# Performance work log

Measured on AMD Instinct MI355X. Metric: run time of the kernel, lower is better.

## Reference

```python
import jax, jax.numpy as jnp
import numpy as np


def setup_inputs() -> dict:
    key = jax.random.key(0)
    ks = jax.random.split(key, 9)
    B, C, H, W = 8, 512, 56, 56
    E = 256  # embed_dim = in_channels / r
    s = 0.02
    return {
        "x": jax.random.normal(ks[0], (B, C, H, W), dtype=jnp.float32),
        "wq": jax.random.normal(ks[1], (E, C), dtype=jnp.float32) * s,
        "bq": jax.random.normal(ks[2], (E,), dtype=jnp.float32) * s,
        "wk": jax.random.normal(ks[3], (E, C), dtype=jnp.float32) * s,
        "bk": jax.random.normal(ks[4], (E,), dtype=jnp.float32) * s,
        "wv": jax.random.normal(ks[5], (E, C), dtype=jnp.float32) * s,
        "bv": jax.random.normal(ks[6], (E,), dtype=jnp.float32) * s,
        "wo": jax.random.normal(ks[7], (C, E), dtype=jnp.float32) * s,
        "bo": jax.random.normal(ks[8], (C,), dtype=jnp.float32) * s,
    }


def reference(x, wq, bq, wk, bk, wv, bv, wo, bo):
    B, C, H, W = x.shape
    N = H * W
    # 1x1 convs == per-pixel linear projections; flatten spatial dims
    xf = x.reshape(B, C, N)                                   # b c n
    q = jnp.einsum("ec,bcn->bne", wq, xf) + bq                # b n e
    k = jnp.einsum("ec,bcn->ben", wk, xf) + bk[None, :, None] # b e n
    v = jnp.einsum("ec,bcn->bne", wv, xf) + bv                # b n e
    attn = jnp.einsum("bne,bem->bnm", q, k) / N               # b n n (unnormalized, /N scale)
    embed = jnp.einsum("bnm,bme->bne", attn, v)               # b n e
    out = jnp.einsum("ce,bne->bcn", wo, embed) + bo[None, :, None]
    return out.reshape(B, C, H, W) + x
```

## Files before the change

### kernel.cpp

```cpp
#include <hip/hip_runtime.h>
#include <hip/hip_bf16.h>


typedef __attribute__((ext_vector_type(8))) __bf16 bf16x8;
typedef __attribute__((ext_vector_type(4))) float floatx4;

struct __align__(8) bh4 { __hip_bfloat16 x, y, z, w; };
struct __align__(16) bh8 { __hip_bfloat16 h[8]; };

__device__ __forceinline__ void load_lds16(const void* g, void* l) {
    __builtin_amdgcn_global_load_lds((const __attribute__((address_space(1))) void*)g,
                                     (__attribute__((address_space(3))) void*)l, 16, 0, 0);
}

__global__ __launch_bounds__(256)
void prep_trans(const float* __restrict__ x, __hip_bfloat16* __restrict__ xT,
                __hip_bfloat16* __restrict__ xnp, float* __restrict__ s,
                const float* __restrict__ wo, const float* __restrict__ wv,
                const float* __restrict__ wq, const float* __restrict__ wk,
                const float* __restrict__ bq, const float* __restrict__ bk,
                const float* __restrict__ bv,
                __hip_bfloat16* __restrict__ Pdb, __hip_bfloat16* __restrict__ Qtb,
                float* __restrict__ u, float* __restrict__ r, float* __restrict__ w,
                float* __restrict__ kap)
{
    __shared__ __align__(16) float smem[64 * 65];
    const int tid = threadIdx.x;

    if (blockIdx.z == 8) {
        const int blk = blockIdx.y * 50 + blockIdx.x;
        if (blk >= 131) return;
        if (blk >= 128) {
            int blk2 = blk - 128;
            if (blk2 < 2) {
                int c = blk2 * 256 + tid;
                float su = 0.f, sr = 0.f, sw = 0.f;
                for (int e = 0; e < 256; ++e) {
                    su = fmaf(wo[(long long)c * 256 + e], bv[e], su);
                    sr = fmaf(bk[e], wq[(long long)e * 512 + c], sr);
                    sw = fmaf(wk[(long long)e * 512 + c], bq[e], sw);
                }
                u[c] = su; r[c] = sr; w[c] = sw;
                if (c == 0) {
                    float k2 = 0.f;
                    for (int e = 0; e < 256; ++e) k2 = fmaf(bk[e], bq[e], k2);
                    *kap = k2;
                }
            } else {
                float4* p = (float4*)s;
                for (int i = tid; i < 1024; i += 256) p[i] = make_float4(0.f, 0.f, 0.f, 0.f);
            }
            return;
        }
        const bool doQ = (blk >= 64);
        const int tt = blk & 63;
        const int m0 = (tt >> 3) * 64, n0 = (tt & 7) * 64;
        float (*As)[68] = (float(*)[68])smem;
        float (*Bs)[68] = (float(*)[68])(smem + 16 * 68);
        const int tx = tid & 15, ty = tid >> 4;
        const int lk = tid >> 4, lc = (tid & 15) * 4;
        const int lr = tid >> 2, lk4 = (tid & 3) * 4;
        float acc[4][4] = {};
        for (int k0 = 0; k0 < 256; k0 += 16) {
            float4 av, bv4;
            if (doQ) {
                av = *(const float4*)&wq[(long long)(k0 + lk) * 512 + m0 + lc];
                bv4 = *(const float4*)&wk[(long long)(k0 + lk) * 512 + n0 + lc];
            } else {
                av = *(const float4*)&wo[(long long)(m0 + lr) * 256 + k0 + lk4];
                bv4 = *(const float4*)&wv[(long long)(k0 + lk) * 512 + n0 + lc];
            }
            __syncthreads();
            if (doQ) {
                *(float4*)&As[lk][lc] = av;
            } else {
                As[lk4 + 0][lr] = av.x; As[lk4 + 1][lr] = av.y;
                As[lk4 + 2][lr] = av.z; As[lk4 + 3][lr] = av.w;
            }
            *(float4*)&Bs[lk][lc] = bv4;
            __syncthreads();
#pragma unroll
            for (int kk = 0; kk < 16; ++kk) {
                float a[4], b[4];
#pragma unroll
                for (int i = 0; i < 4; ++i) { a[i] = As[kk][ty * 4 + i]; b[i] = Bs[kk][tx * 4 + i]; }
#pragma unroll
                for (int i = 0; i < 4; ++i)
#pragma unroll
                    for (int j = 0; j < 4; ++j) acc[i][j] = fmaf(a[i], b[j], acc[i][j]);
            }
        }
        const int mo = m0 + ty * 4, no = n0 + tx * 4;
        if (doQ) {
#pragma unroll
            for (int i = 0; i < 4; ++i)
#pragma unroll
                for (int j = 0; j < 4; ++j)
                    Qtb[(long long)(mo + i) * 512 + no + j] = __float2bfloat16(acc[i][j]);
        } else {
#pragma unroll
            for (int i = 0; i < 4; ++i)
#pragma unroll
                for (int j = 0; j < 4; ++j) {
                    __hip_bfloat16 v = __float2bfloat16(acc[i][j]);
                    Pdb[(long long)(mo + i) * 1024 + no + j] = v;
                    Pdb[(long long)(mo + i) * 1024 + no + j + 512] = v;
                }
        }
        return;
    }

    float (*t)[65] = (float(*)[65])smem;
    const int b = blockIdx.z;
    const int n0 = blockIdx.x * 64, c0 = blockIdx.y * 64;
    const int nch = tid & 7;
    const int cr  = tid >> 3;
    __hip_bfloat16* xTo = xT + (long long)b * 3200 * 512;
    __hip_bfloat16* xno = xnp + (long long)b * 512 * 3200;

    if (n0 >= 3136) {
        bh8 z8;
#pragma unroll
        for (int k = 0; k < 8; ++k) z8.h[k] = __float2bfloat16(0.f);
#pragma unroll
        for (int pass = 0; pass < 2; ++pass) {
            int rr = cr + 32 * pass;
            *(bh8*)&xno[(long long)(c0 + rr) * 3200 + n0 + nch * 8] = z8;
            *(bh8*)&xTo[(long long)(n0 + rr) * 512 + c0 + nch * 8] = z8;
        }
        return;
    }
    const float* xb = x + (long long)b * 512 * 3136;
#pragma unroll
    for (int pass = 0; pass < 2; ++pass) {
        const int cl = cr + 32 * pass;
        const int c = c0 + cl;
        const float* xr = xb + (long long)c * 3136 + n0 + nch * 8;
        float4 v0 = *(const float4*)xr;
        float4 v1 = *(const float4*)(xr + 4);
        bh8 o;
        o.h[0] = __float2bfloat16(v0.x); o.h[1] = __float2bfloat16(v0.y);
        o.h[2] = __float2bfloat16(v0.z); o.h[3] = __float2bfloat16(v0.w);
        o.h[4] = __float2bfloat16(v1.x); o.h[5] = __float2bfloat16(v1.y);
        o.h[6] = __float2bfloat16(v1.z); o.h[7] = __float2bfloat16(v1.w);
        *(bh8*)&xno[(long long)c * 3200 + n0 + nch * 8] = o;
        const int nl = nch * 8;
        t[nl + 0][cl] = v0.x; t[nl + 1][cl] = v0.y;
        t[nl + 2][cl] = v0.z; t[nl + 3][cl] = v0.w;
        t[nl + 4][cl] = v1.x; t[nl + 5][cl] = v1.y;
        t[nl + 6][cl] = v1.z; t[nl + 7][cl] = v1.w;
        float rs = v0.x + v0.y + v0.z + v0.w + v1.x + v1.y + v1.z + v1.w;
        rs += __shfl_xor(rs, 1, 8);
        rs += __shfl_xor(rs, 2, 8);
        rs += __shfl_xor(rs, 4, 8);
        if (nch == 0) atomicAdd(&s[b * 512 + c], rs);
    }
    __syncthreads();
#pragma unroll
    for (int pass = 0; pass < 2; ++pass) {
        const int nl = cr + 32 * pass;
        const int cc = nch * 8;
        bh8 o;
#pragma unroll
        for (int k = 0; k < 8; ++k) o.h[k] = __float2bfloat16(t[nl][cc + k]);
        *(bh8*)&xTo[(long long)(n0 + nl) * 512 + c0 + cc] = o;
    }
}

__global__ __launch_bounds__(256)
void vec2_kernel(const __hip_bfloat16* __restrict__ T, const __hip_bfloat16* __restrict__ Pdb,
                 const __hip_bfloat16* __restrict__ Qtb, const float* __restrict__ s,
                 const float* __restrict__ u, const float* __restrict__ w,
                 const float* __restrict__ kap, const float* __restrict__ bo,
                 float* __restrict__ ps, float* __restrict__ sq, float* __restrict__ a2)
{
    const int idx = blockIdx.x * 4 + (threadIdx.x >> 6);
    const int lane = threadIdx.x & 63;
    const int b = idx >> 9, c = idx & 511;
    const int j0 = lane * 8;
    const float* sb = s + b * 512;
    float4 s0 = *(const float4*)&sb[j0], s1 = *(const float4*)&sb[j0 + 4];
    float4 w0 = *(const float4*)&w[j0],  w1 = *(const float4*)&w[j0 + 4];
    bf16x8 pv = *(const bf16x8*)&Pdb[(long long)c * 1024 + j0];
    bf16x8 qv = *(const bf16x8*)&Qtb[(long long)c * 512 + j0];
    bf16x8 tv = *(const bf16x8*)&T[(long long)b * 262144 + (long long)c * 512 + j0];
    float sj[8] = {s0.x, s0.y, s0.z, s0.w, s1.x, s1.y, s1.z, s1.w};
    float wj[8] = {w0.x, w0.y, w0.z, w0.w, w1.x, w1.y, w1.z, w1.w};
    float aps = 0.f, asq = 0.f, atw = 0.f, asw = 0.f;
#pragma unroll
    for (int t = 0; t < 8; ++t) {
        aps = fmaf((float)pv[t], sj[t], aps);
        asq = fmaf((float)qv[t], sj[t], asq);
        atw = fmaf((float)tv[t], wj[t], atw);
        asw = fmaf(sj[t], wj[t], asw);
    }
#pragma unroll
    for (int m = 1; m < 64; m <<= 1) {
        aps += __shfl_xor(aps, m);
        asq += __shfl_xor(asq, m);
        atw += __shfl_xor(atw, m);
        asw += __shfl_xor(asw, m);
    }
    if (lane == 0) {
        ps[idx] = aps; sq[idx] = asq;
        float kp = *kap;
        a2[idx] = (atw + u[c] * asw + aps * kp) * (1.f / 3136.f) + u[c] * kp + bo[c];
    }
}

#define SWZ64(row) ((row) & 7)

__global__ __launch_bounds__(256)
void mfma_g(const __hip_bfloat16* __restrict__ A, long long sA, int lda,
            __hip_bfloat16* __restrict__ C, long long sC, int ldc,
            int kLen)
{
    constexpr int BKT = 64;
    constexpr int CPR = BKT / 8;
    constexpr int NC = 64 * CPR / 256;
    constexpr int LSZ = 64 * BKT;
    __shared__ __hip_bfloat16 As[2 * LSZ];
    __shared__ __hip_bfloat16 Bs[2 * LSZ];
    const int tid = threadIdx.x;
    const int lane = tid & 63;
    const int w = tid >> 6;
    const int wm = (w >> 1) << 5;
    const int wn = (w & 1) << 5;
    const int ln = lane & 15;
    const int hi = lane >> 4;
    const int bx = blockIdx.x;
    const int batch = bx & 7, ks = bx >> 3;
    int p = blockIdx.y, mt = 0;
    while (p >= 8 - mt) { p -= 8 - mt; ++mt; }
    const int nt = mt + p;
    const int m0 = mt << 6, n0 = nt << 6;
    const long long k0 = (long long)ks * kLen;

    const __hip_bfloat16* gA[NC];
    const __hip_bfloat16* gB[NC];
#pragma unroll
    for (int q0 = 0; q0 < NC; ++q0) {
        int q = tid + 256 * q0;
        int row = q / CPR;
        int c = (q % CPR) ^ SWZ64(row);
        gA[q0] = A + batch * sA + (long long)(m0 + row) * lda + k0 + c * 8;
        gB[q0] = A + batch * sA + (long long)(n0 + row) * lda + k0 + c * 8;
    }
    floatx4 acc[2][2] = {};
    const int nK = kLen / BKT;

#pragma unroll
    for (int q0 = 0; q0 < NC; ++q0) {
        load_lds16(gA[q0], As + (tid + 256 * q0) * 8);
        load_lds16(gB[q0], Bs + (tid + 256 * q0) * 8);
        gA[q0] += BKT; gB[q0] += BKT;
    }

    int cur = 0;
    for (int kt = 0; kt < nK; ++kt) {
        if (kt + 1 < nK) {
            const int off = (cur ^ 1) * LSZ;
#pragma unroll
            for (int q0 = 0; q0 < NC; ++q0) {
                load_lds16(gA[q0], As + off + (tid + 256 * q0) * 8);
                load_lds16(gB[q0], Bs + off + (tid + 256 * q0) * 8);
                gA[q0] += BKT; gB[q0] += BKT;
            }
            asm volatile("s_waitcnt vmcnt(4)" ::: "memory");
        } else {
            asm volatile("s_waitcnt vmcnt(0)" ::: "memory");
        }
        __builtin_amdgcn_s_barrier();
        const __hip_bfloat16* Ac = As + cur * LSZ;
        const __hip_bfloat16* Bc = Bs + cur * LSZ;
#pragma unroll
        for (int kk = 0; kk < BKT / 32; ++kk) {
            const int cidx = kk * 4 + hi;
            bf16x8 af[2], bfr[2];
#pragma unroll
            for (int i = 0; i < 2; ++i) {
                int row = wm + i * 16 + ln;
                af[i] = *(const bf16x8*)(Ac + row * BKT + ((cidx ^ SWZ64(row)) << 3));
            }
#pragma unroll
            for (int j = 0; j < 2; ++j) {
                int row = wn + j * 16 + ln;
                bfr[j] = *(const bf16x8*)(Bc + row * BKT + ((cidx ^ SWZ64(row)) << 3));
            }
#pragma unroll
            for (int i = 0; i < 2; ++i)
#pragma unroll
                for (int j = 0; j < 2; ++j)
                    acc[i][j] = __builtin_amdgcn_mfma_f32_16x16x32_bf16(af[i], bfr[j], acc[i][j], 0, 0, 0);
        }
        if (kt + 1 < nK) {
            __builtin_amdgcn_s_barrier();
            cur ^= 1;
        }
    }

    __hip_bfloat16* Cb = C + batch * sC + ks * 512;
#pragma unroll
    for (int i = 0; i < 2; ++i) {
        int mb = m0 + wm + i * 16 + hi * 4;
#pragma unroll
        for (int j = 0; j < 2; ++j) {
            int nl = n0 + wn + j * 16 + ln;
            bh4 mv;
            mv.x = __float2bfloat16(acc[i][j][0]);
            mv.y = __float2bfloat16(acc[i][j][1]);
            mv.z = __float2bfloat16(acc[i][j][2]);
            mv.w = __float2bfloat16(acc[i][j][3]);
            Cb[(long long)(mb + 0) * ldc + nl] = mv.x;
            Cb[(long long)(mb + 1) * ldc + nl] = mv.y;
            Cb[(long long)(mb + 2) * ldc + nl] = mv.z;
            Cb[(long long)(mb + 3) * ldc + nl] = mv.w;
            if (mt != nt)
                *(bh4*)&Cb[(long long)nl * ldc + mb] = mv;
        }
    }
}

template<int MODE>
__global__ __launch_bounds__(256)
void mfma_sm(const __hip_bfloat16* __restrict__ A, long long sA, int lda,
             const __hip_bfloat16* __restrict__ B, long long sB, int ldb,
             __hip_bfloat16* __restrict__ C, long long sC, int ldc,
             const float* __restrict__ pu, const float* __restrict__ pr,
             const float* __restrict__ pps, const float* __restrict__ psq,
             int kLen)
{
    constexpr int BKT = 64;
    constexpr int CPR = BKT / 8;
    constexpr int NC = 64 * CPR / 256;
    constexpr int LSZ = 64 * BKT;
    __shared__ __hip_bfloat16 As[2 * LSZ];
    __shared__ __hip_bfloat16 Bs[2 * LSZ];
    const int tid = threadIdx.x;
    const int lane = tid & 63;
    const int w = tid >> 6;
    const int wm = (w >> 1) << 5;
    const int wn = (w & 1) << 5;
    const int ln = lane & 15;
    const int hi = lane >> 4;
    const int batch = blockIdx.x;
    const int m0 = blockIdx.z << 6;
    const int n0 = blockIdx.y << 6;

    const __hip_bfloat16* gA[NC];
    const __hip_bfloat16* gB[NC];
#pragma unroll
    for (int q0 = 0; q0 < NC; ++q0) {
        int q = tid + 256 * q0;
        int row = q / CPR;
        int c = (q % CPR) ^ SWZ64(row);
        gA[q0] = A + batch * sA + (long long)(m0 + row) * lda + c * 8;
        gB[q0] = B + batch * sB + (long long)(n0 + row) * ldb + c * 8;
    }
    floatx4 acc[2][2] = {};
    const int nK = kLen / BKT;

#pragma unroll
    for (int q0 = 0; q0 < NC; ++q0) {
        load_lds16(gA[q0], As + (tid + 256 * q0) * 8);
        load_lds16(gB[q0], Bs + (tid + 256 * q0) * 8);
        gA[q0] += BKT; gB[q0] += BKT;
    }

    int cur = 0;
    for (int kt = 0; kt < nK; ++kt) {
        if (kt + 1 < nK) {
            const int off = (cur ^ 1) * LSZ;
#pragma unroll
            for (int q0 = 0; q0 < NC; ++q0) {
                load_lds16(gA[q0], As + off + (tid + 256 * q0) * 8);
                load_lds16(gB[q0], Bs + off + (tid + 256 * q0) * 8);
                gA[q0] += BKT; gB[q0] += BKT;
            }
            asm volatile("s_waitcnt vmcnt(4)" ::: "memory");
        } else {
            asm volatile("s_waitcnt vmcnt(0)" ::: "memory");
        }
        __builtin_amdgcn_s_barrier();
        const __hip_bfloat16* Ac = As + cur * LSZ;
        const __hip_bfloat16* Bc = Bs + cur * LSZ;
#pragma unroll
        for (int kk = 0; kk < BKT / 32; ++kk) {
            const int cidx = kk * 4 + hi;
            bf16x8 af[2], bfr[2];
#pragma unroll
            for (int i = 0; i < 2; ++i) {
                int row = wm + i * 16 + ln;
                af[i] = *(const bf16x8*)(Ac + row * BKT + ((cidx ^ SWZ64(row)) << 3));
            }
#pragma unroll
            for (int j = 0; j < 2; ++j) {
                int row = wn + j * 16 + ln;
                bfr[j] = *(const bf16x8*)(Bc + row * BKT + ((cidx ^ SWZ64(row)) << 3));
            }
#pragma unroll
            for (int i = 0; i < 2; ++i)
#pragma unroll
                for (int j = 0; j < 2; ++j)
                    acc[i][j] = __builtin_amdgcn_mfma_f32_16x16x32_bf16(af[i], bfr[j], acc[i][j], 0, 0, 0);
        }
        if (kt + 1 < nK) {
            __builtin_amdgcn_s_barrier();
            cur ^= 1;
        }
    }

    __hip_bfloat16* Cb = C + batch * sC;
#pragma unroll
    for (int i = 0; i < 2; ++i) {
        int mb = m0 + wm + i * 16 + hi * 4;
#pragma unroll
        for (int r = 0; r < 4; ++r) {
#pragma unroll
            for (int j = 0; j < 2; ++j) {
                int nl = n0 + wn + j * 16 + ln;
                float v = acc[i][j][r];
                if (MODE == 6) {
                    float uu = pu[mb + r], rr = pr[nl];
                    v = (v + uu * psq[batch * 512 + nl] + pps[batch * 512 + mb + r] * rr)
                        * (1.f / 3136.f) + uu * rr;
                    if (mb + r == nl) v += 1.f;
                }
                Cb[(long long)(mb + r) * ldc + nl] = __float2bfloat16(v);
            }
        }
    }
}

__global__ __launch_bounds__(256)
void mfma64(const __hip_bfloat16* __restrict__ A, long long sA, int lda,
            const __hip_bfloat16* __restrict__ B, long long sB, int ldb,
            float* __restrict__ C, long long sC, int ldc,
            const float* __restrict__ bias, int sBias,
            int kLen, int Nreal)
{
    constexpr int BKT = 64;
    constexpr int CPR = BKT / 8;
    constexpr int NA = 64 * CPR / 256;
    constexpr int NB = 128 * CPR / 256;
    __shared__ __hip_bfloat16 As[64 * BKT];
    __shared__ __hip_bfloat16 Bs[128 * BKT];
    const int tid = threadIdx.x;
    const int lane = tid & 63;
    const int w = tid >> 6;
    const int ln = lane & 15;
    const int hi = lane >> 4;
    const int batch = blockIdx.x;
    const int m0 = blockIdx.z << 6;
    const int n0 = blockIdx.y << 7;

    const __hip_bfloat16* gA[NA];
    const __hip_bfloat16* gB[NB];
#pragma unroll
    for (int q0 = 0; q0 < NA; ++q0) {
        int q = tid + 256 * q0;
        int row = q / CPR;
        int c = (q % CPR) ^ SWZ64(row);
        gA[q0] = A + batch * sA + (long long)(m0 + row) * lda + c * 8;
    }
#pragma unroll
    for (int q0 = 0; q0 < NB; ++q0) {
        int q = tid + 256 * q0;
        int row = q / CPR;
        int c = (q % CPR) ^ SWZ64(row);
        gB[q0] = B + batch * sB + (long long)(n0 + row) * ldb + c * 8;
    }

    floatx4 acc[4][2] = {};
    const int nK = kLen / BKT;
    for (int kt = 0; kt < nK; ++kt) {
#pragma unroll
        for (int q0 = 0; q0 < NA; ++q0) {
            load_lds16(gA[q0], As + (tid + 256 * q0) * 8);
            gA[q0] += BKT;
        }
#pragma unroll
        for (int q0 = 0; q0 < NB; ++q0) {
            load_lds16(gB[q0], Bs + (tid + 256 * q0) * 8);
            gB[q0] += BKT;
        }
        __syncthreads();
#pragma unroll
        for (int kk = 0; kk < BKT / 32; ++kk) {
            const int cidx = kk * 4 + hi;
            bf16x8 af[4], bfr[2];
#pragma unroll
            for (int i = 0; i < 4; ++i) {
                int row = i * 16 + ln;
                af[i] = *(const bf16x8*)(As + row * BKT + ((cidx ^ SWZ64(row)) << 3));
            }
#pragma unroll
            for (int j = 0; j < 2; ++j) {
                int row = w * 32 + j * 16 + ln;
                bfr[j] = *(const bf16x8*)(Bs + row * BKT + ((cidx ^ SWZ64(row)) << 3));
            }
#pragma unroll
            for (int i = 0; i < 4; ++i)
#pragma unroll
                for (int j = 0; j < 2; ++j)
                    acc[i][j] = __builtin_amdgcn_mfma_f32_16x16x32_bf16(af[i], bfr[j], acc[i][j], 0, 0, 0);
        }
        __syncthreads();
    }

    float* Cb = C + batch * sC;
#pragma unroll
    for (int i = 0; i < 4; ++i) {
        int mb = m0 + i * 16 + hi * 4;
#pragma unroll
        for (int r = 0; r < 4; ++r) {
            float bb = bias[batch * sBias + mb + r];
#pragma unroll
            for (int j = 0; j < 2; ++j) {
                int nl = n0 + w * 32 + j * 16 + ln;
                if (nl < Nreal) {
                    Cb[(long long)(mb + r) * ldc + nl] = acc[i][j][r] + bb;
                }
            }
        }
    }
}

extern "C" void kernel_launch(void* const* d_in, const int* in_sizes, int n_in,
                              void* d_out, int out_size, void* d_ws, size_t ws_size,
                              hipStream_t stream)
{
    const float* x  = (const float*)d_in[0];
    const float* wq = (const float*)d_in[1];
    const float* bq = (const float*)d_in[2];
    const float* wk = (const float*)d_in[3];
    const float* bk = (const float*)d_in[4];
    const float* wv = (const float*)d_in[5];
    const float* bv = (const float*)d_in[6];
    const float* wo = (const float*)d_in[7];
    const float* bo = (const float*)d_in[8];
    float* out = (float*)d_out;

    const int N = 3136;
    const long long xs = 512LL * N;
    const long long xs2 = 512LL * 3200;

    char* ob = (char*)d_out;
    __hip_bfloat16* xnp = (__hip_bfloat16*)ob;
    __hip_bfloat16* Gp2 = (__hip_bfloat16*)(ob + 26214400);
    __hip_bfloat16* Tb  = (__hip_bfloat16*)(ob + 34603008);

    char* wsb = (char*)d_ws;
    __hip_bfloat16* xT  = (__hip_bfloat16*)wsb;
    __hip_bfloat16* A2b = (__hip_bfloat16*)(wsb + 26214400);
    __hip_bfloat16* Pdb = (__hip_bfloat16*)(wsb + 30408704);
    __hip_bfloat16* Qtb = (__hip_bfloat16*)(wsb + 31457280);
    float* sv  = (float*)(wsb + 31981568);
    float* u_  = (float*)(wsb + 31997952);
    float* r_  = (float*)(wsb + 32000000);
    float* w_  = (float*)(wsb + 32002048);
    float* kap = (float*)(wsb + 32004096);
    float* ps  = (float*)(wsb + 32004112);
    float* sq  = (float*)(wsb + 32020496);
    float* a2v = (float*)(wsb + 32036880);

    prep_trans<<<dim3(50, 8, 9), 256, 0, stream>>>(
        x, xT, xnp, sv, wo, wv, wq, wk, bq, bk, bv,
        Pdb, Qtb, u_, r_, w_, kap);

    mfma_g<<<dim3(16, 36), 256, 0, stream>>>(
        xnp, xs2, 3200, Gp2, 524288, 1024, 1600);

    mfma_sm<5><<<dim3(8, 8, 8), 256, 0, stream>>>(
        Pdb, 0, 1024, Gp2, 524288, 1024, Tb, 262144, 512,
        nullptr, nullptr, nullptr, nullptr, 1024);

    vec2_kernel<<<1024, 256, 0, stream>>>(Tb, Pdb, Qtb, sv, u_, w_, kap, bo, ps, sq, a2v);

    mfma_sm<6><<<dim3(8, 8, 8), 256, 0, stream>>>(
        Tb, 262144, 512, Qtb, 0, 512, A2b, 262144, 512,
        u_, r_, ps, sq, 512);

    mfma64<<<dim3(8, 25, 8), 256, 0, stream>>>(
        A2b, 262144, 512, xT, 3200LL * 512, 512,
        out, xs, N, a2v, 512, 512, N);
}
```

Before: 212.8 us.

## Drop transposed x copy; transpose B tile in LDS inside final GEMM

The prep kernel no longer writes a transposed bf16 copy of x (xT), which removes one full-size write of about 26MB and its LDS transpose. The final GEMM now reads the channel-major xnp buffer directly, using register loads and scalar short stores into LDS with a new swizzle instead of async global-to-LDS loads. The zeroing of the row-sum buffer moves from an extra prep block to a hipMemsetAsync, and xnp is relocated into the workspace. The trade-off is a slower B-tile fill in the GEMM: eight scattered 2-byte LDS stores per vector, with possible bank conflicts, and no asynchronous load path.

```diff
diff --git a/kernel.cpp b/kernel.cpp
--- a/kernel.cpp
+++ b/kernel.cpp
@@ -3,6 +3,7 @@
 
 
 typedef __attribute__((ext_vector_type(8))) __bf16 bf16x8;
+typedef __attribute__((ext_vector_type(8))) short s16x8;
 typedef __attribute__((ext_vector_type(4))) float floatx4;
 
 struct __align__(8) bh4 { __hip_bfloat16 x, y, z, w; };
@@ -14,8 +15,8 @@
 }
 
 __global__ __launch_bounds__(256)
-void prep_trans(const float* __restrict__ x, __hip_bfloat16* __restrict__ xT,
-                __hip_bfloat16* __restrict__ xnp, float* __restrict__ s,
+void prep_trans(const float* __restrict__ x, __hip_bfloat16* __restrict__ xnp,
+                float* __restrict__ s,
                 const float* __restrict__ wo, const float* __restrict__ wv,
                 const float* __restrict__ wq, const float* __restrict__ wk,
                 const float* __restrict__ bq, const float* __restrict__ bk,
@@ -24,31 +25,25 @@
                 float* __restrict__ u, float* __restrict__ r, float* __restrict__ w,
                 float* __restrict__ kap)
 {
-    __shared__ __align__(16) float smem[64 * 65];
+    __shared__ __align__(16) float smem[2 * 16 * 68];
     const int tid = threadIdx.x;
 
     if (blockIdx.z == 8) {
         const int blk = blockIdx.y * 50 + blockIdx.x;
-        if (blk >= 131) return;
+        if (blk >= 130) return;
         if (blk >= 128) {
-            int blk2 = blk - 128;
-            if (blk2 < 2) {
-                int c = blk2 * 256 + tid;
-                float su = 0.f, sr = 0.f, sw = 0.f;
-                for (int e = 0; e < 256; ++e) {
-                    su = fmaf(wo[(long long)c * 256 + e], bv[e], su);
-                    sr = fmaf(bk[e], wq[(long long)e * 512 + c], sr);
-                    sw = fmaf(wk[(long long)e * 512 + c], bq[e], sw);
-                }
-                u[c] = su; r[c] = sr; w[c] = sw;
-                if (c == 0) {
-                    float k2 = 0.f;
-                    for (int e = 0; e < 256; ++e) k2 = fmaf(bk[e], bq[e], k2);
-                    *kap = k2;
-                }
-            } else {
-                float4* p = (float4*)s;
-                for (int i = tid; i < 1024; i += 256) p[i] = make_float4(0.f, 0.f, 0.f, 0.f);
+            int c = (blk - 128) * 256 + tid;
+            float su = 0.f, sr = 0.f, sw = 0.f;
+            for (int e = 0; e < 256; ++e) {
+                su = fmaf(wo[(long long)c * 256 + e], bv[e], su);
+                sr = fmaf(bk[e], wq[(long long)e * 512 + c], sr);
+                sw = fmaf(wk[(long long)e * 512 + c], bq[e], sw);
+            }
+            u[c] = su; r[c] = sr; w[c] = sw;
+            if (c == 0) {
+                float k2 = 0.f;
+                for (int e = 0; e < 256; ++e) k2 = fmaf(bk[e], bq[e], k2);
+                *kap = k2;
             }
             return;
         }
@@ -110,12 +105,10 @@
         return;
     }
 
-    float (*t)[65] = (float(*)[65])smem;
     const int b = blockIdx.z;
     const int n0 = blockIdx.x * 64, c0 = blockIdx.y * 64;
     const int nch = tid & 7;
     const int cr  = tid >> 3;
-    __hip_bfloat16* xTo = xT + (long long)b * 3200 * 512;
     __hip_bfloat16* xno = xnp + (long long)b * 512 * 3200;
 
     if (n0 >= 3136) {
@@ -123,47 +116,37 @@
 #pragma unroll
         for (int k = 0; k < 8; ++k) z8.h[k] = __float2bfloat16(0.f);
 #pragma unroll
-        for (int pass = 0; pass < 2; ++pass) {
-            int rr = cr + 32 * pass;
-            *(bh8*)&xno[(long long)(c0 + rr) * 3200 + n0 + nch * 8] = z8;
-            *(bh8*)&xTo[(long long)(n0 + rr) * 512 + c0 + nch * 8] = z8;
-        }
+        for (int p = 0; p < 2; ++p)
+            *(bh8*)&xno[(long long)(c0 + cr + 32 * p) * 3200 + n0 + nch * 8] = z8;
         return;
     }
     const float* xb = x + (long long)b * 512 * 3136;
-#pragma unroll
-    for (int pass = 0; pass < 2; ++pass) {
-        const int cl = cr + 32 * pass;
-        const int c = c0 + cl;
-        const float* xr = xb + (long long)c * 3136 + n0 + nch * 8;
-        float4 v0 = *(const float4*)xr;
-        float4 v1 = *(const float4*)(xr + 4);
+    float4 v[2][2];
+#pragma unroll
+    for (int p = 0; p < 2; ++p) {
+        const float* xr = xb + (long long)(c0 + cr + 32 * p) * 3136 + n0 + nch * 8;
+        v[p][0] = *(const float4*)xr;
+        v[p][1] = *(const float4*)(xr + 4);
+    }
+    float rsum[2];
+#pragma unroll
+    for (int p = 0; p < 2; ++p) {
+        float4 v0 = v[p][0], v1 = v[p][1];
         bh8 o;
         o.h[0] = __float2bfloat16(v0.x); o.h[1] = __float2bfloat16(v0.y);
         o.h[2] = __float2bfloat16(v0.z); o.h[3] = __float2bfloat16(v0.w);
         o.h[4] = __float2bfloat16(v1.x); o.h[5] = __float2bfloat16(v1.y);
         o.h[6] = __float2bfloat16(v1.z); o.h[7] = __float2bfloat16(v1.w);
-        *(bh8*)&xno[(long long)c * 3200 + n0 + nch * 8] = o;
-        const int nl = nch * 8;
-        t[nl + 0][cl] = v0.x; t[nl + 1][cl] = v0.y;
-        t[nl + 2][cl] = v0.z; t[nl + 3][cl] = v0.w;
-        t[nl + 4][cl] = v1.x; t[nl + 5][cl] = v1.y;
-        t[nl + 6][cl] = v1.z; t[nl + 7][cl] = v1.w;
+        *(bh8*)&xno[(long long)(c0 + cr + 32 * p) * 3200 + n0 + nch * 8] = o;
         float rs = v0.x + v0.y + v0.z + v0.w + v1.x + v1.y + v1.z + v1.w;
         rs += __shfl_xor(rs, 1, 8);
         rs += __shfl_xor(rs, 2, 8);
         rs += __shfl_xor(rs, 4, 8);
-        if (nch == 0) atomicAdd(&s[b * 512 + c], rs);
-    }
-    __syncthreads();
-#pragma unroll
-    for (int pass = 0; pass < 2; ++pass) {
-        const int nl = cr + 32 * pass;
-        const int cc = nch * 8;
-        bh8 o;
-#pragma unroll
-        for (int k = 0; k < 8; ++k) o.h[k] = __float2bfloat16(t[nl][cc + k]);
-        *(bh8*)&xTo[(long long)(n0 + nl) * 512 + c0 + cc] = o;
+        rsum[p] = rs;
+    }
+    if (nch == 0) {
+        atomicAdd(&s[b * 512 + c0 + cr], rsum[0]);
+        atomicAdd(&s[b * 512 + c0 + cr + 32], rsum[1]);
     }
 }
 
@@ -432,9 +415,11 @@
     }
 }
 
+#define SWZB(nr) (((nr) & 7) ^ (((nr) >> 3) & 7))
+
 __global__ __launch_bounds__(256)
 void mfma64(const __hip_bfloat16* __restrict__ A, long long sA, int lda,
-            const __hip_bfloat16* __restrict__ B, long long sB, int ldb,
+            const __hip_bfloat16* __restrict__ Bn, long long sB, int ldb,
             float* __restrict__ C, long long sC, int ldc,
             const float* __restrict__ bias, int sBias,
             int kLen, int Nreal)
@@ -442,9 +427,8 @@
     constexpr int BKT = 64;
     constexpr int CPR = BKT / 8;
     constexpr int NA = 64 * CPR / 256;
-    constexpr int NB = 128 * CPR / 256;
     __shared__ __hip_bfloat16 As[64 * BKT];
-    __shared__ __hip_bfloat16 Bs[128 * BKT];
+    __shared__ __align__(16) short Bs[128 * 64];
     const int tid = threadIdx.x;
     const int lane = tid & 63;
     const int w = tid >> 6;
@@ -455,7 +439,6 @@
     const int n0 = blockIdx.y << 7;
 
     const __hip_bfloat16* gA[NA];
-    const __hip_bfloat16* gB[NB];
 #pragma unroll
     for (int q0 = 0; q0 < NA; ++q0) {
         int q = tid + 256 * q0;
@@ -463,26 +446,33 @@
         int c = (q % CPR) ^ SWZ64(row);
         gA[q0] = A + batch * sA + (long long)(m0 + row) * lda + c * 8;
     }
-#pragma unroll
-    for (int q0 = 0; q0 < NB; ++q0) {
-        int q = tid + 256 * q0;
-        int row = q / CPR;
-        int c = (q % CPR) ^ SWZ64(row);
-        gB[q0] = B + batch * sB + (long long)(n0 + row) * ldb + c * 8;
-    }
+    const int bc = tid >> 2;
+    const int bq = tid & 3;
+    const short* bbase = (const short*)(Bn + batch * sB)
+                         + (long long)bc * ldb + n0 + bq * 8;
+    const int g = bc >> 3;
 
     floatx4 acc[4][2] = {};
     const int nK = kLen / BKT;
     for (int kt = 0; kt < nK; ++kt) {
+        s16x8 vb[4];
+        const short* bp = bbase + (long long)kt * 64 * ldb;
+#pragma unroll
+        for (int m = 0; m < 4; ++m)
+            vb[m] = *(const s16x8*)(bp + m * 32);
 #pragma unroll
         for (int q0 = 0; q0 < NA; ++q0) {
             load_lds16(gA[q0], As + (tid + 256 * q0) * 8);
             gA[q0] += BKT;
         }
 #pragma unroll
-        for (int q0 = 0; q0 < NB; ++q0) {
-            load_lds16(gB[q0], Bs + (tid + 256 * q0) * 8);
-            gB[q0] += BKT;
+        for (int m = 0; m < 4; ++m) {
+            const int nb = (bq + 4 * m) * 8;
+#pragma unroll
+            for (int k = 0; k < 8; ++k) {
+                const int nr = nb + k;
+                Bs[nr * 64 + (((g ^ SWZB(nr)) & 7) << 3) + (bc & 7)] = vb[m][k];
+            }
         }
         __syncthreads();
 #pragma unroll
@@ -497,7 +487,8 @@
 #pragma unroll
             for (int j = 0; j < 2; ++j) {
                 int row = w * 32 + j * 16 + ln;
-                bfr[j] = *(const bf16x8*)(Bs + row * BKT + ((cidx ^ SWZ64(row)) << 3));
+                bfr[j] = *(const bf16x8*)((const __hip_bfloat16*)Bs
+                          + row * 64 + (((cidx ^ SWZB(row)) & 7) << 3));
             }
 #pragma unroll
             for (int i = 0; i < 4; ++i)
@@ -546,12 +537,11 @@
     const long long xs2 = 512LL * 3200;
 
     char* ob = (char*)d_out;
-    __hip_bfloat16* xnp = (__hip_bfloat16*)ob;
     __hip_bfloat16* Gp2 = (__hip_bfloat16*)(ob + 26214400);
     __hip_bfloat16* Tb  = (__hip_bfloat16*)(ob + 34603008);
 
     char* wsb = (char*)d_ws;
-    __hip_bfloat16* xT  = (__hip_bfloat16*)wsb;
+    __hip_bfloat16* xnp = (__hip_bfloat16*)wsb;
     __hip_bfloat16* A2b = (__hip_bfloat16*)(wsb + 26214400);
     __hip_bfloat16* Pdb = (__hip_bfloat16*)(wsb + 30408704);
     __hip_bfloat16* Qtb = (__hip_bfloat16*)(wsb + 31457280);
@@ -564,8 +554,10 @@
     float* sq  = (float*)(wsb + 32020496);
     float* a2v = (float*)(wsb + 32036880);
 
+    hipMemsetAsync(sv, 0, 512 * 8 * sizeof(float), stream);
+
     prep_trans<<<dim3(50, 8, 9), 256, 0, stream>>>(
-        x, xT, xnp, sv, wo, wv, wq, wk, bq, bk, bv,
+        x, xnp, sv, wo, wv, wq, wk, bq, bk, bv,
         Pdb, Qtb, u_, r_, w_, kap);
 
     mfma_g<<<dim3(16, 36), 256, 0, stream>>>(
@@ -582,6 +574,6 @@
         u_, r_, ps, sq, 512);
 
     mfma64<<<dim3(8, 25, 8), 256, 0, stream>>>(
-        A2b, 262144, 512, xT, 3200LL * 512, 512,
+        A2b, 262144, 512, xnp, xs2, 3200,
         out, xs, N, a2v, 512, 512, N);
 }
```

Measured after the change: 215.7 us. No clear change (+1.3%).
